# Optimization experiments

Hardware: AMD Instinct MI355X
Metric: run time of the kernel (lower is better)

## Reference

```python
import jax, jax.numpy as jnp
import numpy as np

EPS = 1e-06
K = 32


def setup_inputs() -> dict:
    key = jax.random.key(0)
    k1, k2, k3, k4, k5 = jax.random.split(key, 5)
    d_model, n_latents = 1024, 16384
    x = jax.random.normal(k1, (2, 2048, d_model), dtype=jnp.float32)
    b_pre = jax.random.normal(k2, (d_model,), dtype=jnp.float32) * 0.02
    W_enc = jax.random.normal(k3, (n_latents, d_model), dtype=jnp.float32) / np.sqrt(d_model)
    b_enc = jax.random.normal(k4, (n_latents,), dtype=jnp.float32) * 0.02
    W_dec = jax.random.normal(k5, (d_model, n_latents), dtype=jnp.float32)
    # mimic normalize_decoder_weights: unit norm along dim=1 (n_latents axis per row)
    W_dec = W_dec / jnp.linalg.norm(W_dec, axis=1, keepdims=True)
    return {"x": x, "b_pre": b_pre, "W_enc": W_enc, "b_enc": b_enc, "W_dec": W_dec}


def reference(x, b_pre, W_enc, b_enc, W_dec):
    B, S, D = x.shape
    # preprocess: center + normalize (torch .std is unbiased, ddof=1)
    mean = jnp.mean(x, axis=-1, keepdims=True)
    norm = jnp.std(x, axis=-1, keepdims=True, ddof=1) + EPS
    xn = ((x - mean) / norm).reshape(-1, D)          # [N, D]
    # encode
    h = (xn - b_pre) @ W_enc.T + b_enc               # [N, n_latents]
    # top-k + relu + scatter into sparse latent
    vals, idx = jax.lax.top_k(h, K)                  # [N, K]
    vals = jax.nn.relu(vals)
    rows = jnp.arange(h.shape[0])[:, None]
    h_sparse = jnp.zeros_like(h).at[rows, idx].set(vals)
    # decode (dense matmul over mostly-zero latents, as in the original)
    recon = h_sparse @ W_dec.T + b_pre               # [N, D]
    # postprocess: denormalize
    recon = recon.reshape(B, S, D) * norm + mean
    return recon
```

## Files before the change

kernel.cpp:

```cpp
#include <hip/hip_runtime.h>
#include <cstdint>
#include <cstddef>

typedef _Float16 half_t;
typedef _Float16 half4_t __attribute__((ext_vector_type(4)));
typedef _Float16 half8_t __attribute__((ext_vector_type(8)));
typedef unsigned short ushort8_t __attribute__((ext_vector_type(8)));
typedef float floatx4 __attribute__((ext_vector_type(4)));

#define NROWS 4096
#define DMODEL 1024
#define NLAT 16384
#define CAND_MAX 256

#define MBYTE (1ull << 20)
static const size_t oW0    = 0;
static const size_t oWdT   = 32 * MBYTE;
static const size_t oMeanD = 64 * MBYTE;
static const size_t oNormD = 64 * MBYTE + (64ull << 10);
static const size_t oBatch = 65 * MBYTE;

#define BATCH_ROW_BYTES 34816ull

__device__ __forceinline__ void gload16(const void* g, void* l) {
  __builtin_amdgcn_global_load_lds(
      (const __attribute__((address_space(1))) void*)g,
      (__attribute__((address_space(3))) void*)l, 16, 0, 0);
}

#define WSPLIT_B 2048
#define TRANS_B  4096
__global__ __launch_bounds__(256) void prepro_kernel(
    const float* __restrict__ x, const float* __restrict__ b_pre,
    const float* __restrict__ W_enc, const float* __restrict__ Wd,
    half_t* __restrict__ W0h, half_t* __restrict__ WdT,
    half_t* __restrict__ X0,
    double* __restrict__ meanD, double* __restrict__ normD, int r0) {
  int bid = blockIdx.x, tid = threadIdx.x;
  if (bid < WSPLIT_B) {
    size_t base = (size_t)bid * 2048 + tid;
    for (int it = 0; it < 8; ++it) {
      size_t i = base + (size_t)it * 256;
      float4 v = ((const float4*)W_enc)[i];
      half4_t h0;
      h0[0] = (half_t)(v.x * 1024.0f);
      h0[1] = (half_t)(v.y * 1024.0f);
      h0[2] = (half_t)(v.z * 1024.0f);
      h0[3] = (half_t)(v.w * 1024.0f);
      ((half4_t*)W0h)[i] = h0;
    }
    return;
  }
  if (bid < WSPLIT_B + TRANS_B) {
    __shared__ float tile[64][65];
    int t = bid - WSPLIT_B;
    int c0 = (t & 255) * 64;
    int r0t = (t >> 8) * 64;
    int tc = tid & 63, tg = tid >> 6;
    for (int i = 0; i < 16; ++i) {
      int rr = i * 4 + tg;
      tile[rr][tc] = Wd[(size_t)(r0t + rr) * NLAT + c0 + tc];
    }
    __syncthreads();
    for (int i = 0; i < 16; ++i) {
      int cc = i * 4 + tg;
      WdT[(size_t)(c0 + cc) * DMODEL + r0t + tc] = (half_t)tile[tc][cc];
    }
    return;
  }
  int rl = bid - WSPLIT_B - TRANS_B;
  int rg = r0 + rl;
  const float4* px = (const float4*)(x + (size_t)rg * DMODEL);
  float4 v = px[tid];
  double s  = (double)v.x + (double)v.y + (double)v.z + (double)v.w;
  double sq = (double)v.x * v.x + (double)v.y * v.y +
              (double)v.z * v.z + (double)v.w * v.w;
  for (int off = 32; off; off >>= 1) {
    s += __shfl_down(s, off);
    sq += __shfl_down(sq, off);
  }
  __shared__ double ss[4], ssq[4];
  __shared__ double sMean, sNorm;
  int wv = tid >> 6, ln = tid & 63;
  if (ln == 0) { ss[wv] = s; ssq[wv] = sq; }
  __syncthreads();
  if (tid == 0) {
    double S = ss[0] + ss[1] + ss[2] + ss[3];
    double Q = ssq[0] + ssq[1] + ssq[2] + ssq[3];
    double mean = S / (double)DMODEL;
    double var = (Q - (double)DMODEL * mean * mean) / (double)(DMODEL - 1);
    double nrm = sqrt(var) + 1e-6;
    sMean = mean; sNorm = nrm;
    meanD[rg] = mean; normD[rg] = nrm;
  }
  __syncthreads();
  float mean = (float)sMean, nrm = (float)sNorm;
  const float4* pb = (const float4*)b_pre;
  float4 bp = pb[tid];
  float c[4];
  c[0] = ((v.x - mean) / nrm - bp.x) * 1024.0f;
  c[1] = ((v.y - mean) / nrm - bp.y) * 1024.0f;
  c[2] = ((v.z - mean) / nrm - bp.z) * 1024.0f;
  c[3] = ((v.w - mean) / nrm - bp.w) * 1024.0f;
  half4_t h0;
  for (int i = 0; i < 4; ++i) h0[i] = (half_t)c[i];
  ((half4_t*)(X0 + (size_t)rl * DMODEL))[tid] = h0;
}

__global__ __launch_bounds__(512, 2) void gemm_enc(
    const half_t* __restrict__ X0, const half_t* __restrict__ W0,
    const float* __restrict__ b_enc, half_t* __restrict__ h, int mtiles) {
  __shared__ __align__(16) half_t As[2][256 * 64];
  __shared__ __align__(16) half_t Bs[2][256 * 64];
  int tid = threadIdx.x;
  int lane = tid & 63, wave = tid >> 6;
  int wm = wave >> 2, wn = wave & 3;

  int bid = blockIdx.x;
  int xcd = bid & 7, q = bid >> 3;
  int bn = xcd * 8 + (q & 7);
  int bm = q >> 3;
  (void)mtiles;

  const char* Ag = (const char*)(X0 + (size_t)bm * 256 * DMODEL);
  const char* Bg = (const char*)(W0 + (size_t)bn * 256 * DMODEL);

  int srcSwz = ((lane & 7) ^ (lane >> 3)) << 4;
  int rowBase = wave * 8 + (lane >> 3);
  int ldsWOff = wave * 1024;

#define STG_A(b, kt, pr) { int colB = ((kt) & 15) * 128 + srcSwz;             \
    gload16(Ag + (size_t)((pr) * 64 + rowBase) * 2048 + colB,                 \
            (char*)As[b] + (pr) * 8192 + ldsWOff);                            \
    gload16(Ag + (size_t)(((pr) + 2) * 64 + rowBase) * 2048 + colB,           \
            (char*)As[b] + ((pr) + 2) * 8192 + ldsWOff); }
#define STG_B(b, kt, pr) { int colB = ((kt) & 15) * 128 + srcSwz;             \
    gload16(Bg + (size_t)((pr) * 64 + rowBase) * 2048 + colB,                 \
            (char*)Bs[b] + (pr) * 8192 + ldsWOff);                            \
    gload16(Bg + (size_t)(((pr) + 2) * 64 + rowBase) * 2048 + colB,           \
            (char*)Bs[b] + ((pr) + 2) * 8192 + ldsWOff); }

  floatx4 acc[8][4] = {};

  STG_B(0, 0, 0); STG_B(0, 0, 1); STG_A(0, 0, 0); STG_A(0, 0, 1);
  STG_B(1, 1, 0); STG_B(1, 1, 1); STG_A(1, 1, 0);
  asm volatile("s_waitcnt vmcnt(6)" ::: "memory");
  __builtin_amdgcn_sched_barrier(0);
  __builtin_amdgcn_s_barrier();

  int laneQ = (lane & 15) * 128 + (lane >> 4) * 16;
  int sxor = (lane & 7) << 4;
  int aRow = wm * 128 * 128;
  int bRow = wn * 64 * 128;

  half8_t bfr[2][4], afA[4], afB[4];
  const char *Ab, *Bb;

#define LD_B(kk) _Pragma("unroll") for (int t = 0; t < 4; ++t)                \
    bfr[kk][t] = *(const half8_t*)(Bb + ((bRow + t * 2048 +                   \
                                          (kk) * 64 + laneQ) ^ sxor));
#define LD_AF(DST, mh, kk) _Pragma("unroll") for (int t = 0; t < 4; ++t)      \
    DST[t] = *(const half8_t*)(Ab + ((aRow + ((mh) * 4 + t) * 2048 +          \
                                      (kk) * 64 + laneQ) ^ sxor));
#define MM(mb, FR, kk) __builtin_amdgcn_s_setprio(1);                         \
    _Pragma("unroll") for (int mi = 0; mi < 4; ++mi)                          \
    _Pragma("unroll") for (int ni = 0; ni < 4; ++ni)                          \
      acc[(mb) + mi][ni] = __builtin_amdgcn_mfma_f32_16x16x32_f16(            \
          FR[mi], bfr[kk][ni], acc[(mb) + mi][ni], 0, 0, 0);                  \
    __builtin_amdgcn_s_setprio(0);
#define BAR() __builtin_amdgcn_s_barrier()
#define LGKM(n) { asm volatile("s_waitcnt lgkmcnt(" #n ")" ::: "memory");     \
    __builtin_amdgcn_sched_barrier(0); }
#define VM6() { asm volatile("s_waitcnt vmcnt(6)" ::: "memory");              \
    __builtin_amdgcn_sched_barrier(0); }
#define VM0() { asm volatile("s_waitcnt vmcnt(0)" ::: "memory");              \
    __builtin_amdgcn_sched_barrier(0); }

#pragma unroll 1
  for (int i = 0; i < 7; ++i) {
    int t0 = 2 * i;
    Ab = (const char*)As[0]; Bb = (const char*)Bs[0];
    LD_B(0); LD_B(1); LD_AF(afA, 0, 0); LD_AF(afB, 1, 0);
    STG_A(1, t0 + 1, 1);
    BAR(); LGKM(4); MM(0, afA, 0); BAR();
    LD_AF(afA, 0, 1);
    STG_B(0, t0 + 2, 0);
    BAR(); LGKM(4); MM(4, afB, 0); BAR();
    LD_AF(afB, 1, 1);
    STG_B(0, t0 + 2, 1);
    BAR(); LGKM(4); MM(0, afA, 1); BAR();
    STG_A(0, t0 + 2, 0);
    BAR(); LGKM(0); MM(4, afB, 1); VM6(); BAR();
    Ab = (const char*)As[1]; Bb = (const char*)Bs[1];
    LD_B(0); LD_B(1); LD_AF(afA, 0, 0); LD_AF(afB, 1, 0);
    STG_A(0, t0 + 2, 1);
    BAR(); LGKM(4); MM(0, afA, 0); BAR();
    LD_AF(afA, 0, 1);
    STG_B(1, t0 + 3, 0);
    BAR(); LGKM(4); MM(4, afB, 0); BAR();
    LD_AF(afB, 1, 1);
    STG_B(1, t0 + 3, 1);
    BAR(); LGKM(4); MM(0, afA, 1); BAR();
    STG_A(1, t0 + 3, 0);
    BAR(); LGKM(0); MM(4, afB, 1); VM6(); BAR();
  }
  {
    Ab = (const char*)As[0]; Bb = (const char*)Bs[0];
    LD_B(0); LD_B(1); LD_AF(afA, 0, 0); LD_AF(afB, 1, 0);
    STG_A(1, 15, 1);
    BAR(); LGKM(4); MM(0, afA, 0); BAR();
    LD_AF(afA, 0, 1);
    BAR(); LGKM(4); MM(4, afB, 0); BAR();
    LD_AF(afB, 1, 1);
    BAR(); LGKM(4); MM(0, afA, 1); BAR();
    BAR(); LGKM(0); MM(4, afB, 1); VM0(); BAR();
    Ab = (const char*)As[1]; Bb = (const char*)Bs[1];
    LD_B(0); LD_B(1); LD_AF(afA, 0, 0); LD_AF(afB, 1, 0);
    LGKM(4); MM(0, afA, 0);
    LD_AF(afA, 0, 1);
    LGKM(4); MM(4, afB, 0);
    LD_AF(afB, 1, 1);
    LGKM(4); MM(0, afA, 1);
    LGKM(0); MM(4, afB, 1);
  }
#undef STG_A
#undef STG_B
#undef LD_B
#undef LD_AF
#undef MM
#undef BAR
#undef LGKM
#undef VM6
#undef VM0

  const float scale = 0x1p-20f;
  int rowb = bm * 256 + wm * 128 + ((lane >> 4) * 4);
  int colb = bn * 256 + wn * 64 + (lane & 15);
  float be[4];
#pragma unroll
  for (int ni = 0; ni < 4; ++ni) be[ni] = b_enc[colb + ni * 16];
#pragma unroll
  for (int mi = 0; mi < 8; ++mi)
#pragma unroll
    for (int ni = 0; ni < 4; ++ni)
#pragma unroll
      for (int r = 0; r < 4; ++r)
        h[(size_t)(rowb + mi * 16 + r) * NLAT + colb + ni * 16] =
            (half_t)(acc[mi][ni][r] * scale + be[ni]);
}

__global__ __launch_bounds__(256) void postproc(
    const half_t* __restrict__ h, const float* __restrict__ x,
    const float* __restrict__ b_pre, const float* __restrict__ W_enc,
    const float* __restrict__ b_enc,
    const double* __restrict__ meanD, const double* __restrict__ normD,
    const half_t* __restrict__ WdT, float* __restrict__ out, int r0) {
  int rl = blockIdx.x, tid = threadIdx.x;
  int rg = r0 + rl;
  int wv = tid >> 6, ln = tid & 63;
  const ushort8_t* ph8 = (const ushort8_t*)(h + (size_t)rl * NLAT);

  __shared__ half_t hrow[NLAT];
  __shared__ float tmax[256];
  __shared__ float sThresh;
  __shared__ int cCount;
  __shared__ int cI[CAND_MAX];
  __shared__ double cV[CAND_MAX];
  __shared__ float sVal[32];
  __shared__ int sIdx[32];

  double mean = meanD[rg], nrm = normD[rg];
  const float* px = x + (size_t)rg * DMODEL;
  double xr[16];
#pragma unroll
  for (int u = 0; u < 16; ++u)
    xr[u] = ((double)px[ln + u * 64] - mean) / nrm - (double)b_pre[ln + u * 64];

  if (tid == 0) cCount = 0;
  float m = -3.4e38f;
  for (int i = 0; i < 8; ++i) {
    ushort8_t v = ph8[tid + i * 256];
    ((ushort8_t*)hrow)[tid + i * 256] = v;
#pragma unroll
    for (int e = 0; e < 8; ++e) {
      float f = (float)__builtin_bit_cast(_Float16, (unsigned short)v[e]);
      m = fmaxf(m, f);
    }
  }
  tmax[tid] = m;
  __syncthreads();

  {
    int rank = 0;
    for (int o = 0; o < 256; ++o) {
      float vo = tmax[o];
      rank += (vo > m || (vo == m && o < tid)) ? 1 : 0;
    }
    if (rank == 31) sThresh = m - 0.02f;
  }
  __syncthreads();
  float thresh = sThresh;

  for (int i = 0; i < 8; ++i) {
    ushort8_t v = ((const ushort8_t*)hrow)[tid + i * 256];
#pragma unroll
    for (int e = 0; e < 8; ++e) {
      float f = (float)__builtin_bit_cast(_Float16, (unsigned short)v[e]);
      if (f >= thresh) {
        int slot = atomicAdd(&cCount, 1);
        if (slot < CAND_MAX) cI[slot] = (tid + i * 256) * 8 + e;
      }
    }
  }
  __syncthreads();
  int nc = (cCount < CAND_MAX) ? cCount : CAND_MAX;

  for (int c0 = wv * 4; c0 < nc; c0 += 16) {
    const float* wp[4];
#pragma unroll
    for (int qq = 0; qq < 4; ++qq) {
      int c = c0 + qq;
      int j = cI[c < nc ? c : (nc - 1)];
      wp[qq] = W_enc + (size_t)j * DMODEL + ln;
    }
    double a0 = 0.0, a1 = 0.0, a2 = 0.0, a3 = 0.0;
#pragma unroll
    for (int u = 0; u < 16; ++u) {
      float w0 = wp[0][u * 64];
      float w1 = wp[1][u * 64];
      float w2 = wp[2][u * 64];
      float w3 = wp[3][u * 64];
      a0 += xr[u] * (double)w0;
      a1 += xr[u] * (double)w1;
      a2 += xr[u] * (double)w2;
      a3 += xr[u] * (double)w3;
    }
    double accq[4] = {a0, a1, a2, a3};
#pragma unroll
    for (int qq = 0; qq < 4; ++qq) {
      double s = accq[qq];
      for (int off = 32; off; off >>= 1) s += __shfl_down(s, off);
      int c = c0 + qq;
      if (ln == 0 && c < nc) cV[c] = s + (double)b_enc[cI[c]];
    }
  }
  if (tid < 32) { sVal[tid] = 0.0f; sIdx[tid] = 0; }
  __syncthreads();

  for (int c = tid; c < nc; c += 256) {
    double v = cV[c];
    int ix = cI[c];
    int rank = 0;
    for (int o = 0; o < nc; ++o) {
      double vo = cV[o];
      int io = cI[o];
      rank += (vo > v || (vo == v && io < ix)) ? 1 : 0;
    }
    if (rank < 32) {
      sIdx[rank] = ix;
      sVal[rank] = (float)(v > 0.0 ? v : 0.0);
    }
  }
  __syncthreads();

  int d0 = tid * 4;
  float4 accv = {0.f, 0.f, 0.f, 0.f};
#pragma unroll 8
  for (int k = 0; k < 32; ++k) {
    float vk = sVal[k];
    const half4_t wvv = *(const half4_t*)(WdT + (size_t)sIdx[k] * DMODEL + d0);
    accv.x += vk * (float)wvv[0]; accv.y += vk * (float)wvv[1];
    accv.z += vk * (float)wvv[2]; accv.w += vk * (float)wvv[3];
  }
  float4 bp = ((const float4*)b_pre)[tid];
  float nrmf = (float)nrm, mnf = (float)mean;
  float4 o;
  o.x = (accv.x + bp.x) * nrmf + mnf;
  o.y = (accv.y + bp.y) * nrmf + mnf;
  o.z = (accv.z + bp.z) * nrmf + mnf;
  o.w = (accv.w + bp.w) * nrmf + mnf;
  ((float4*)(out + (size_t)rg * DMODEL))[tid] = o;
}

extern "C" void kernel_launch(void* const* d_in, const int* in_sizes, int n_in,
                              void* d_out, int out_size, void* d_ws, size_t ws_size,
                              hipStream_t stream) {
  const float* x     = (const float*)d_in[0];
  const float* b_pre = (const float*)d_in[1];
  const float* W_enc = (const float*)d_in[2];
  const float* b_enc = (const float*)d_in[3];
  const float* W_dec = (const float*)d_in[4];
  float* out = (float*)d_out;
  char* ws = (char*)d_ws;

  int rowsB = NROWS;
  while (rowsB > 256) {
    size_t need = oBatch + (size_t)rowsB * BATCH_ROW_BYTES;
    if (need <= ws_size) break;
    rowsB >>= 1;
  }
  if (oBatch + (size_t)rowsB * BATCH_ROW_BYTES > ws_size) return;

  half_t* W0 = (half_t*)(ws + oW0);
  half_t* WdT = (half_t*)(ws + oWdT);
  double* meanD = (double*)(ws + oMeanD);
  double* normD = (double*)(ws + oNormD);
  half_t* X0b  = (half_t*)(ws + oBatch);
  half_t* hb   = X0b + (size_t)rowsB * DMODEL;

  for (int r0 = 0; r0 < NROWS; r0 += rowsB) {
    hipLaunchKernelGGL(prepro_kernel,
                       dim3(WSPLIT_B + TRANS_B + rowsB), dim3(256), 0, stream,
                       x, b_pre, W_enc, W_dec, W0, WdT, X0b, meanD, normD, r0);
    int mtiles = rowsB / 256;
    hipLaunchKernelGGL(gemm_enc, dim3(mtiles * 64), dim3(512), 0, stream,
                       X0b, W0, b_enc, hb, mtiles);
    hipLaunchKernelGGL(postproc, dim3(rowsB), dim3(256), 0, stream,
                       hb, x, b_pre, W_enc, b_enc, meanD, normD, WdT, out, r0);
  }
}
```

Before: 329.8 us.

## Widen postproc to 512 threads with vectorized float4 rescoring loads

The postproc kernel now launches 512 threads per row instead of 256. The wider block splits the row max scan, candidate rescoring across 8 waves, and the 32-term decode, which is divided into two halves combined through shared memory. The x, b_pre and W_enc reads in the double-precision rescoring switch from strided scalar loads to float4 loads, which changes how elements map to lanes. This adds parallelism and memory-load efficiency per row, at the cost of more shared memory, an extra barrier, and a 512-entry rank scan for the threshold.

```diff
diff --git a/kernel.cpp b/kernel.cpp
--- a/kernel.cpp
+++ b/kernel.cpp
@@ -249,7 +249,7 @@
             (half_t)(acc[mi][ni][r] * scale + be[ni]);
 }
 
-__global__ __launch_bounds__(256) void postproc(
+__global__ __launch_bounds__(512, 4) void postproc(
     const half_t* __restrict__ h, const float* __restrict__ x,
     const float* __restrict__ b_pre, const float* __restrict__ W_enc,
     const float* __restrict__ b_enc,
@@ -261,26 +261,33 @@
   const ushort8_t* ph8 = (const ushort8_t*)(h + (size_t)rl * NLAT);
 
   __shared__ half_t hrow[NLAT];
-  __shared__ float tmax[256];
+  __shared__ float tmax[512];
   __shared__ float sThresh;
   __shared__ int cCount;
   __shared__ int cI[CAND_MAX];
   __shared__ double cV[CAND_MAX];
   __shared__ float sVal[32];
   __shared__ int sIdx[32];
+  __shared__ float4 sAcc[256];
 
   double mean = meanD[rg], nrm = normD[rg];
   const float* px = x + (size_t)rg * DMODEL;
   double xr[16];
 #pragma unroll
-  for (int u = 0; u < 16; ++u)
-    xr[u] = ((double)px[ln + u * 64] - mean) / nrm - (double)b_pre[ln + u * 64];
+  for (int s = 0; s < 4; ++s) {
+    float4 xv = *(const float4*)(px + s * 256 + 4 * ln);
+    float4 bv = *(const float4*)(b_pre + s * 256 + 4 * ln);
+    xr[s * 4 + 0] = ((double)xv.x - mean) / nrm - (double)bv.x;
+    xr[s * 4 + 1] = ((double)xv.y - mean) / nrm - (double)bv.y;
+    xr[s * 4 + 2] = ((double)xv.z - mean) / nrm - (double)bv.z;
+    xr[s * 4 + 3] = ((double)xv.w - mean) / nrm - (double)bv.w;
+  }
 
   if (tid == 0) cCount = 0;
   float m = -3.4e38f;
-  for (int i = 0; i < 8; ++i) {
-    ushort8_t v = ph8[tid + i * 256];
-    ((ushort8_t*)hrow)[tid + i * 256] = v;
+  for (int i = 0; i < 4; ++i) {
+    ushort8_t v = ph8[tid + i * 512];
+    ((ushort8_t*)hrow)[tid + i * 512] = v;
 #pragma unroll
     for (int e = 0; e < 8; ++e) {
       float f = (float)__builtin_bit_cast(_Float16, (unsigned short)v[e]);
@@ -292,7 +299,7 @@
 
   {
     int rank = 0;
-    for (int o = 0; o < 256; ++o) {
+    for (int o = 0; o < 512; ++o) {
       float vo = tmax[o];
       rank += (vo > m || (vo == m && o < tid)) ? 1 : 0;
     }
@@ -301,39 +308,43 @@
   __syncthreads();
   float thresh = sThresh;
 
-  for (int i = 0; i < 8; ++i) {
-    ushort8_t v = ((const ushort8_t*)hrow)[tid + i * 256];
+  for (int i = 0; i < 4; ++i) {
+    ushort8_t v = ((const ushort8_t*)hrow)[tid + i * 512];
 #pragma unroll
     for (int e = 0; e < 8; ++e) {
       float f = (float)__builtin_bit_cast(_Float16, (unsigned short)v[e]);
       if (f >= thresh) {
         int slot = atomicAdd(&cCount, 1);
-        if (slot < CAND_MAX) cI[slot] = (tid + i * 256) * 8 + e;
+        if (slot < CAND_MAX) cI[slot] = (tid + i * 512) * 8 + e;
       }
     }
   }
   __syncthreads();
   int nc = (cCount < CAND_MAX) ? cCount : CAND_MAX;
 
-  for (int c0 = wv * 4; c0 < nc; c0 += 16) {
-    const float* wp[4];
+  for (int c0 = wv * 4; c0 < nc; c0 += 32) {
+    const char* wp[4];
 #pragma unroll
     for (int qq = 0; qq < 4; ++qq) {
       int c = c0 + qq;
       int j = cI[c < nc ? c : (nc - 1)];
-      wp[qq] = W_enc + (size_t)j * DMODEL + ln;
+      wp[qq] = (const char*)(W_enc + (size_t)j * DMODEL) + 16 * ln;
     }
     double a0 = 0.0, a1 = 0.0, a2 = 0.0, a3 = 0.0;
 #pragma unroll
-    for (int u = 0; u < 16; ++u) {
-      float w0 = wp[0][u * 64];
-      float w1 = wp[1][u * 64];
-      float w2 = wp[2][u * 64];
-      float w3 = wp[3][u * 64];
-      a0 += xr[u] * (double)w0;
-      a1 += xr[u] * (double)w1;
-      a2 += xr[u] * (double)w2;
-      a3 += xr[u] * (double)w3;
+    for (int s = 0; s < 4; ++s) {
+      float4 w0 = *(const float4*)(wp[0] + s * 1024);
+      float4 w1 = *(const float4*)(wp[1] + s * 1024);
+      float4 w2 = *(const float4*)(wp[2] + s * 1024);
+      float4 w3 = *(const float4*)(wp[3] + s * 1024);
+      a0 += xr[s*4+0]*(double)w0.x + xr[s*4+1]*(double)w0.y +
+            xr[s*4+2]*(double)w0.z + xr[s*4+3]*(double)w0.w;
+      a1 += xr[s*4+0]*(double)w1.x + xr[s*4+1]*(double)w1.y +
+            xr[s*4+2]*(double)w1.z + xr[s*4+3]*(double)w1.w;
+      a2 += xr[s*4+0]*(double)w2.x + xr[s*4+1]*(double)w2.y +
+            xr[s*4+2]*(double)w2.z + xr[s*4+3]*(double)w2.w;
+      a3 += xr[s*4+0]*(double)w3.x + xr[s*4+1]*(double)w3.y +
+            xr[s*4+2]*(double)w3.z + xr[s*4+3]*(double)w3.w;
     }
     double accq[4] = {a0, a1, a2, a3};
 #pragma unroll
@@ -347,7 +358,7 @@
   if (tid < 32) { sVal[tid] = 0.0f; sIdx[tid] = 0; }
   __syncthreads();
 
-  for (int c = tid; c < nc; c += 256) {
+  for (int c = tid; c < nc; c += 512) {
     double v = cV[c];
     int ix = cI[c];
     int rank = 0;
@@ -363,23 +374,31 @@
   }
   __syncthreads();
 
-  int d0 = tid * 4;
+  int dt = tid & 255;
+  int d0 = dt * 4;
+  int klo = (tid < 256) ? 0 : 16;
   float4 accv = {0.f, 0.f, 0.f, 0.f};
 #pragma unroll 8
-  for (int k = 0; k < 32; ++k) {
+  for (int k = klo; k < klo + 16; ++k) {
     float vk = sVal[k];
     const half4_t wvv = *(const half4_t*)(WdT + (size_t)sIdx[k] * DMODEL + d0);
     accv.x += vk * (float)wvv[0]; accv.y += vk * (float)wvv[1];
     accv.z += vk * (float)wvv[2]; accv.w += vk * (float)wvv[3];
   }
-  float4 bp = ((const float4*)b_pre)[tid];
-  float nrmf = (float)nrm, mnf = (float)mean;
-  float4 o;
-  o.x = (accv.x + bp.x) * nrmf + mnf;
-  o.y = (accv.y + bp.y) * nrmf + mnf;
-  o.z = (accv.z + bp.z) * nrmf + mnf;
-  o.w = (accv.w + bp.w) * nrmf + mnf;
-  ((float4*)(out + (size_t)rg * DMODEL))[tid] = o;
+  if (tid >= 256) sAcc[dt] = accv;
+  __syncthreads();
+  if (tid < 256) {
+    float4 p = sAcc[dt];
+    accv.x += p.x; accv.y += p.y; accv.z += p.z; accv.w += p.w;
+    float4 bp = ((const float4*)b_pre)[dt];
+    float nrmf = (float)nrm, mnf = (float)mean;
+    float4 o;
+    o.x = (accv.x + bp.x) * nrmf + mnf;
+    o.y = (accv.y + bp.y) * nrmf + mnf;
+    o.z = (accv.z + bp.z) * nrmf + mnf;
+    o.w = (accv.w + bp.w) * nrmf + mnf;
+    ((float4*)(out + (size_t)rg * DMODEL))[dt] = o;
+  }
 }
 
 extern "C" void kernel_launch(void* const* d_in, const int* in_sizes, int n_in,
@@ -415,7 +434,7 @@
     int mtiles = rowsB / 256;
     hipLaunchKernelGGL(gemm_enc, dim3(mtiles * 64), dim3(512), 0, stream,
                        X0b, W0, b_enc, hb, mtiles);
-    hipLaunchKernelGGL(postproc, dim3(rowsB), dim3(256), 0, stream,
+    hipLaunchKernelGGL(postproc, dim3(rowsB), dim3(512), 0, stream,
                        hb, x, b_pre, W_enc, b_enc, meanD, normD, WdT, out, r0);
   }
 }
```

New measurement: 442.9 us. 34.3% more time.
